# Performance work log

Measured on AMD Instinct MI355X. Metric: run time of the kernel, lower is better.

Reference implementation:

```python
import jax, jax.numpy as jnp
import numpy as np

N = 50000
E = 800000
T = 5            # towers
F = 10           # in_num / F_in per tower (divide_input=False)
F_OUT = 2        # out_channels // towers
G = 64           # number of graphs in the batch
L = 2            # conv layers
BN_EPS = 1e-5
STD_EPS = 1e-5


def setup_inputs() -> dict:
    key = jax.random.key(0)
    ks = jax.random.split(key, 24)
    s = 0.1
    inp = {
        'x': jax.random.normal(ks[0], (N, F), jnp.float32),
        'edge_emb': jax.random.normal(ks[1], (4, F), jnp.float32) * s,
        'mlp1_w1': jax.random.normal(ks[2], (F, 5), jnp.float32) * s,
        'mlp1_b1': jnp.zeros((5,), jnp.float32),
        'mlp1_w2': jax.random.normal(ks[3], (5, F), jnp.float32) * s,
        'mlp1_b2': jnp.zeros((F,), jnp.float32),
        'enc_w': jax.random.normal(ks[4], (L, F, F), jnp.float32) * s,
        'enc_b': jnp.zeros((L, F), jnp.float32),
        'pre_w': jax.random.normal(ks[5], (L, T, 3 * F, F), jnp.float32) * s,
        'pre_b': jnp.zeros((L, T, F), jnp.float32),
        'post_w': jax.random.normal(ks[6], (L, T, 13 * F, F_OUT), jnp.float32) * s,
        'post_b': jnp.zeros((L, T, F_OUT), jnp.float32),
        'lin_w': jax.random.normal(ks[7], (L, F, F), jnp.float32) * s,
        'lin_b': jnp.zeros((L, F), jnp.float32),
        'bn_gamma': jnp.ones((L, F), jnp.float32),
        'bn_beta': jnp.zeros((L, F), jnp.float32),
        'mlp2_w1': jax.random.normal(ks[8], (F, 5), jnp.float32) * s,
        'mlp2_b1': jnp.zeros((5,), jnp.float32),
        'mlp2_w2': jax.random.normal(ks[9], (5, 1), jnp.float32) * s,
        'mlp2_b2': jnp.zeros((1,), jnp.float32),
        'edge_index': jax.random.randint(ks[10], (2, E), 0, N, jnp.int64),
        'edge_attr': jax.random.randint(ks[11], (E,), 0, 4, jnp.int64),
        'batch': jnp.sort(jax.random.randint(ks[12], (N,), 0, G, jnp.int64)),
    }
    return inp


def reference(x, edge_emb, mlp1_w1, mlp1_b1, mlp1_w2, mlp1_b2,
              enc_w, enc_b, pre_w, pre_b, post_w, post_b, lin_w, lin_b,
              bn_gamma, bn_beta, mlp2_w1, mlp2_b1, mlp2_w2, mlp2_b2,
              edge_index, edge_attr, batch):
    src, dst = edge_index[0], edge_index[1]
    # mlp1: 10 -> 5 -> 10
    h = jax.nn.relu(x @ mlp1_w1 + mlp1_b1) @ mlp1_w2 + mlp1_b2  # [N, F]
    ea = edge_emb[edge_attr]  # [E, F] edge embedding lookup

    # in-degree at target nodes, PNA degree statistics
    deg = jax.ops.segment_sum(jnp.ones((src.shape[0],), h.dtype), dst, num_segments=N)
    d = jnp.clip(deg, 1.0)
    avg_log = jnp.mean(jnp.log(deg + 1.0))  # avg_deg['log'] from degree distribution
    log_d = jnp.log(d + 1.0)
    amp = (log_d / avg_log)[:, None, None]
    att = (avg_log / log_d)[:, None, None]
    has_in = (deg > 0)[:, None, None]
    inv_d = (1.0 / d)[:, None, None]

    for l in range(L):
        e = ea @ enc_w[l] + enc_b[l]  # [E, F]
        # message = pre_nn(cat(x_i, x_j, edge_attr)) per tower (x shared across towers)
        msg_in = jnp.concatenate([h[dst], h[src], e], axis=-1)  # [E, 3F]
        m = jnp.einsum('ef,tfo->eto', msg_in, pre_w[l]) + pre_b[l]  # [E, T, F]
        mean = jax.ops.segment_sum(m, dst, num_segments=N) * inv_d
        mean2 = jax.ops.segment_sum(m * m, dst, num_segments=N) * inv_d
        std = jnp.sqrt(jax.nn.relu(mean2 - mean * mean) + STD_EPS)
        mn = jnp.where(has_in, jax.ops.segment_min(m, dst, num_segments=N), 0.0)
        mx = jnp.where(has_in, jax.ops.segment_max(m, dst, num_segments=N), 0.0)
        agg = jnp.concatenate([mean, mn, mx, std], axis=-1)  # [N, T, 4F]
        agg = jnp.concatenate([agg, agg * amp, agg * att], axis=-1)  # [N, T, 12F]
        xt = jnp.broadcast_to(h[:, None, :], (h.shape[0], T, F))
        o = jnp.concatenate([xt, agg], axis=-1)  # [N, T, 13F]
        o = jnp.einsum('ntf,tfo->nto', o, post_w[l]) + post_b[l]  # [N, T, F_OUT]
        o = o.reshape(o.shape[0], T * F_OUT) @ lin_w[l] + lin_b[l]  # [N, F]
        # train-mode BatchNorm over nodes
        mu = jnp.mean(o, axis=0)
        var = jnp.var(o, axis=0)
        o = (o - mu) / jnp.sqrt(var + BN_EPS) * bn_gamma[l] + bn_beta[l]
        h = jax.nn.relu(o)

    g = jax.ops.segment_sum(h, batch, num_segments=G)  # global_add_pool -> [G, F]
    out = jax.nn.relu(g @ mlp2_w1 + mlp2_b1) @ mlp2_w2 + mlp2_b2  # [G, 1]
    return out
```

## Files before the change

kernel.cpp:

```cpp
#include <hip/hip_runtime.h>
#include <hip/hip_fp16.h>
#include <math.h>

#define N_NODES 50000
#define N_EDGES 800000
#define G_GRAPHS 64
#define BSTRIDE 64
#define CPAD 16
#define UROW 64
#define SENPK (N_NODES * 128)

#define WAVE_SYNC() asm volatile("s_waitcnt lgkmcnt(0)" ::: "memory")
#define RFL(v) __builtin_amdgcn_readfirstlane(v)

__global__ void k_zero(int* __restrict__ cnt) {
  int n = blockIdx.x * 256 + threadIdx.x;
  if (n < N_NODES) cnt[n * CPAD] = 0;
}

__global__ __launch_bounds__(256) void k_front(
    const float* __restrict__ x,
    const float* __restrict__ w1, const float* __restrict__ b1,
    const float* __restrict__ w2, const float* __restrict__ b2,
    float* __restrict__ h,
    int* __restrict__ cnt,
    float* __restrict__ bn_part, float* __restrict__ g,
    float* __restrict__ avg_log,
    const float* __restrict__ edge_emb,
    const float* __restrict__ enc_w, const float* __restrict__ enc_b,
    const float* __restrict__ pre_w, float* __restrict__ encm,
    __half* __restrict__ u,
    const int* __restrict__ src, const int* __restrict__ dst,
    const int* __restrict__ attr, int* __restrict__ epk) {
  __shared__ float eo[2][4][10];
  __shared__ float sw[500];
  int tid = threadIdx.x;
  int gid = blockIdx.x * 256 + tid;

  int ed = dst[gid];
  int es = src[gid];
  int ea = attr[gid];
  int rk = atomicAdd(&cnt[ed * CPAD], 1);

  if (gid < 1280) bn_part[gid] = 0.f;
  if (gid < G_GRAPHS * 10) g[gid] = 0.f;
  if (gid == 0) avg_log[0] = 0.f;
  { int z = gid - N_NODES; if (z >= 0 && z < UROW) u[N_NODES * UROW + z] = __float2half(0.f); }

  bool act = gid < N_NODES;
  float hr[10];
  if (act) {
    const float2* xp = (const float2*)(x + gid * 10);
    float xv[10];
#pragma unroll
    for (int k = 0; k < 5; k++) { float2 v = xp[k]; xv[2 * k] = v.x; xv[2 * k + 1] = v.y; }
    float hid[5];
#pragma unroll
    for (int j = 0; j < 5; j++) {
      float a = b1[j];
#pragma unroll
      for (int k = 0; k < 10; k++) a += xv[k] * w1[k * 5 + j];
      hid[j] = fmaxf(a, 0.f);
    }
#pragma unroll
    for (int f = 0; f < 10; f++) {
      float a = b2[f];
#pragma unroll
      for (int j = 0; j < 5; j++) a += hid[j] * w2[j * 10 + f];
      hr[f] = a;
      h[gid * 10 + f] = a;
    }
  }

  for (int j = tid; j < 500; j += 256) {
    int t = j / 100, k = (j / 10) % 10, f = j % 10;
    sw[j] = pre_w[(t * 30 + 10 + k) * 10 + f];
  }

  if (rk < BSTRIDE) epk[ed * BSTRIDE + rk] = es * 128 + ea;

  if (blockIdx.x == 0) {
    for (int i = tid; i < 80; i += 256) {
      int l = i / 40; int a = (i / 10) % 4; int k = i % 10;
      float s = enc_b[l * 10 + k];
      for (int j = 0; j < 10; j++) s += edge_emb[a * 10 + j] * enc_w[(l * 10 + j) * 10 + k];
      eo[l][a][k] = s;
    }
  }
  __syncthreads();
  if (blockIdx.x == 0) {
    for (int i = tid; i < 400; i += 256) {
      int l = i / 200; int a = (i / 50) % 4; int t = (i / 10) % 5; int f = i % 10;
      float s = 0.f;
      for (int k = 0; k < 10; k++) s += eo[l][a][k] * pre_w[((l * 5 + t) * 30 + 20 + k) * 10 + f];
      encm[i] = s;
    }
  }

  if (act) {
    __half2* up = (__half2*)(u + (size_t)gid * UROW);
#pragma unroll
    for (int c0 = 0; c0 < 25; c0++) {
      int ca = 2 * c0, cb = 2 * c0 + 1;
      int ta = ca / 10, fa = ca % 10, tb = cb / 10, fb = cb % 10;
      float a = 0.f, b = 0.f;
#pragma unroll
      for (int k = 0; k < 10; k++) {
        a += hr[k] * sw[ta * 100 + fa + k * 10];
        b += hr[k] * sw[tb * 100 + fb + k * 10];
      }
      up[c0] = __floats2half2_rn(a, b);
    }
  }
}

__global__ void k_avg(const int* __restrict__ cnt, float* __restrict__ avg_log,
                      int* __restrict__ epk) {
  __shared__ float ws[4];
  int tid = threadIdx.x;
  float acc = 0.f;
  for (int n = blockIdx.x * 256 + tid; n < N_NODES; n += gridDim.x * 256) {
    int dg = cnt[n * CPAD];
    acc += __logf((float)dg + 1.f);
    int dd = dg < BSTRIDE ? dg : BSTRIDE;
    int end = dd + 8 < BSTRIDE ? dd + 8 : BSTRIDE;
    for (int j = dd; j < end; j++) epk[n * BSTRIDE + j] = SENPK;
  }
#pragma unroll
  for (int d = 32; d >= 1; d >>= 1) acc += __shfl_down(acc, d, 64);
  if ((tid & 63) == 0) ws[tid >> 6] = acc;
  __syncthreads();
  if (tid == 0) atomicAdd(avg_log, ws[0] + ws[1] + ws[2] + ws[3]);
}

__global__ __launch_bounds__(256) void k_conv(
    const float* __restrict__ h,
    const __half* __restrict__ u,
    const float* __restrict__ pre_w_l,
    const float* __restrict__ pre_b_l,
    const float* __restrict__ post_w_l,
    const float* __restrict__ post_b_l,
    const float* __restrict__ lin_w_l,
    const float* __restrict__ lin_b_l,
    const float* __restrict__ encm_l,
    const int* __restrict__ cnt,
    const int* __restrict__ epk,
    const float* __restrict__ avg_log_p,
    float* __restrict__ o_buf,
    float* __restrict__ bn_part)
{
  __shared__ float sW[1300];
  __shared__ float sLin[100];
  __shared__ float sLb[10];
  __shared__ float sPb[10];
  __shared__ float sP[4][100];
  __shared__ float sO[4][10];
  __shared__ float bnS[10], bnQ[10];

  int tid = threadIdx.x;
  int wid = RFL(tid >> 6);
  int lane = tid & 63;
  for (int i = tid; i < 1300; i += 256) sW[i] = post_w_l[i];
  for (int i = tid; i < 100; i += 256) sLin[i] = lin_w_l[i];
  if (tid < 10) {
    sLb[tid] = lin_b_l[tid];
    sPb[tid] = post_b_l[tid];
    bnS[tid] = 0.f; bnQ[tid] = 0.f;
  }
  __syncthreads();

  int f = lane % 10;
  int t = (lane < 50) ? (lane / 10) : 4;
  int c50 = t * 10 + f;
  const char* ub = (const char*)u;
  int c50_2 = c50 * 2;
  float wdst[10];
#pragma unroll
  for (int k = 0; k < 10; k++) wdst[k] = pre_w_l[(t * 30 + k) * 10 + f];
  float em0 = encm_l[c50];
  float em1 = encm_l[50 + c50];
  float em2 = encm_l[100 + c50];
  float em3 = encm_l[150 + c50];
  float preb = pre_b_l[c50];
  float avg_log = avg_log_p[0] * (1.f / N_NODES);

  int n = blockIdx.x * 4 + wid;
  float bnSv = 0.f, bnQv = 0.f;

#define PRE(US, AS, IDX) { int sp_ = __builtin_amdgcn_readlane(pk, (IDX) & 63); \
    AS = sp_ & 3; \
    US = __half2float(*(const __half*)(ub + (sp_ & ~7) + c50_2)); }
#define PROC(US, AS) { float m_ = ((AS & 2) ? ((AS & 1) ? bem3 : bem2) : ((AS & 1) ? bem1 : bem0)) + US; \
    sum += m_; sq = fmaf(m_, m_, sq); mnv = fminf(mnv, m_); mxv = fmaxf(mxv, m_); }

  if (n < N_NODES) {
    int deg = RFL(cnt[n * CPAD]);
    if (deg > BSTRIDE) deg = BSTRIDE;
    int pk = epk[n * BSTRIDE + lane];

    const float* hn = h + n * 10;
    float2 d0 = *(const float2*)hn;
    float2 d1 = *(const float2*)(hn + 2);
    float2 d2 = *(const float2*)(hn + 4);
    float2 d3 = *(const float2*)(hn + 6);
    float2 d4 = *(const float2*)(hn + 8);
    float xf = hn[f];

    float base = preb
      + d0.x * wdst[0] + d0.y * wdst[1] + d1.x * wdst[2] + d1.y * wdst[3]
      + d2.x * wdst[4] + d2.y * wdst[5] + d3.x * wdst[6] + d3.y * wdst[7]
      + d4.x * wdst[8] + d4.y * wdst[9];
    float bem0 = base + em0, bem1 = base + em1, bem2 = base + em2, bem3 = base + em3;

    float sum = 0.f, sq = 0.f, mnv = INFINITY, mxv = -INFINITY;
    {
      float u0, u1, u2, u3, u4, u5, u6, u7;
      int a0, a1, a2, a3, a4, a5, a6, a7;
      PRE(u0, a0, 0) PRE(u1, a1, 1) PRE(u2, a2, 2) PRE(u3, a3, 3)
      PRE(u4, a4, 4) PRE(u5, a5, 5) PRE(u6, a6, 6) PRE(u7, a7, 7)
      int full = deg & ~7;
      int jb = 0;
      for (; jb < full; jb += 8) {
        PROC(u0, a0) PRE(u0, a0, jb + 8)
        PROC(u1, a1) PRE(u1, a1, jb + 9)
        PROC(u2, a2) PRE(u2, a2, jb + 10)
        PROC(u3, a3) PRE(u3, a3, jb + 11)
        PROC(u4, a4) PRE(u4, a4, jb + 12)
        PROC(u5, a5) PRE(u5, a5, jb + 13)
        PROC(u6, a6) PRE(u6, a6, jb + 14)
        PROC(u7, a7) PRE(u7, a7, jb + 15)
      }
      if (jb + 0 < deg) PROC(u0, a0)
      if (jb + 1 < deg) PROC(u1, a1)
      if (jb + 2 < deg) PROC(u2, a2)
      if (jb + 3 < deg) PROC(u3, a3)
      if (jb + 4 < deg) PROC(u4, a4)
      if (jb + 5 < deg) PROC(u5, a5)
      if (jb + 6 < deg) PROC(u6, a6)
    }

    float degf = (float)deg;
    float d = fmaxf(degf, 1.f);
    float inv = 1.f / d;
    float mean = sum * inv;
    float var = sq * inv - mean * mean;
    float stdv = sqrtf(fmaxf(var, 0.f) + 1e-5f);
    if (deg == 0) { mnv = 0.f; mxv = 0.f; }
    float log_d = logf(d + 1.f);
    float amp = log_d / avg_log;
    float att = avg_log / log_d;

    float vv[13];
    vv[0] = xf;
    vv[1] = mean;       vv[2] = mnv;        vv[3] = mxv;        vv[4] = stdv;
    vv[5] = mean * amp; vv[6] = mnv * amp;  vv[7] = mxv * amp;  vv[8] = stdv * amp;
    vv[9] = mean * att; vv[10] = mnv * att; vv[11] = mxv * att; vv[12] = stdv * att;
    float p0 = 0.f, p1 = 0.f;
#pragma unroll
    for (int j = 0; j < 13; j++) {
      const float2 w = *(const float2*)&sW[t * 260 + (f + 10 * j) * 2];
      p0 += vv[j] * w.x; p1 += vv[j] * w.y;
    }
    if (lane < 50) *(float2*)&sP[wid][c50 * 2] = make_float2(p0, p1);
    WAVE_SYNC();
    if (lane < 10) {
      int tt = lane >> 1, c = lane & 1;
      float o = sPb[lane];
#pragma unroll
      for (int ff = 0; ff < 10; ff++) o += sP[wid][(tt * 10 + ff) * 2 + c];
      sO[wid][lane] = o;
    }
    WAVE_SYNC();
    if (lane < 10) {
      float r = sLb[lane];
#pragma unroll
      for (int j = 0; j < 10; j++) r += sO[wid][j] * sLin[j * 10 + lane];
      o_buf[n * 10 + lane] = r;
      bnSv = r; bnQv = r * r;
    }
  }
#undef PRE
#undef PROC

  if (lane < 10) {
    atomicAdd(&bnS[lane], bnSv);
    atomicAdd(&bnQ[lane], bnQv);
  }
  __syncthreads();
  if (tid < 20) {
    float v = (tid < 10) ? bnS[tid] : bnQ[tid - 10];
    atomicAdd(&bn_part[(blockIdx.x & 31) * 20 + tid], v);
  }
}

__global__ __launch_bounds__(256) void k_bnpool(
    const float* __restrict__ o_buf,
    const float* __restrict__ bn_part,
    const float* __restrict__ gamma, const float* __restrict__ beta,
    float* __restrict__ h,
    const int* __restrict__ batch, float* __restrict__ g,
    const float* __restrict__ pre_w_next, __half* __restrict__ u,
    int do_u, int do_pool) {
  __shared__ float sS[20];
  __shared__ float sMu[10], sInv[10];
  __shared__ float pool[8][10];
  __shared__ float hrow[25][10];
  __shared__ float sw[500];
  __shared__ int g0s;
  int tid = threadIdx.x;
  int n0 = blockIdx.x * 25;
  if (do_u) {
    for (int j = tid; j < 500; j += 256) {
      int t = j / 100, k = (j / 10) % 10, f = j % 10;
      sw[j] = pre_w_next[(t * 30 + 10 + k) * 10 + f];
    }
  }
  if (tid < 20) {
    float s = 0.f;
    for (int j = 0; j < 32; j++) s += bn_part[j * 20 + tid];
    sS[tid] = s;
  }
  if (tid < 80) pool[tid / 10][tid % 10] = 0.f;
  if (tid == 0) g0s = batch[n0];
  __syncthreads();
  if (tid < 10) {
    float mu = sS[tid] * (1.f / N_NODES);
    float var = sS[10 + tid] * (1.f / N_NODES) - mu * mu;
    sMu[tid] = mu;
    sInv[tid] = 1.f / sqrtf(fmaxf(var, 0.f) + 1e-5f);
  }
  __syncthreads();
  if (tid < 250) {
    int dn = tid / 10, f = tid % 10;
    int n = n0 + dn;
    int i = n * 10 + f;
    float o = (o_buf[i] - sMu[f]) * sInv[f] * gamma[f] + beta[f];
    float r = fmaxf(o, 0.f);
    h[i] = r;
    hrow[dn][f] = r;
    if (do_pool) {
      int dg = batch[n] - g0s;
      if (dg < 8) atomicAdd(&pool[dg][f], r);
      else atomicAdd(&g[(g0s + dg) * 10 + f], r);
    }
  }
  __syncthreads();
  if (do_u && tid < 250) {
#pragma unroll
    for (int it = 0; it < 5; it++) {
      int j = tid + it * 250;
      int node = j / 50, c = j % 50;
      int t = c / 10, f2 = c % 10;
      float acc = 0.f;
#pragma unroll
      for (int k = 0; k < 10; k++) acc += hrow[node][k] * sw[t * 100 + f2 + k * 10];
      u[(size_t)(n0 + node) * UROW + c] = __float2half_rn(acc);
    }
  }
  if (do_pool) {
    __syncthreads();
    if (tid < 80) {
      float v = pool[tid / 10][tid % 10];
      if (v != 0.f) atomicAdd(&g[(g0s + tid / 10) * 10 + tid % 10], v);
    }
  }
}

__global__ void k_mlp2(const float* __restrict__ g,
                       const float* __restrict__ w1, const float* __restrict__ b1,
                       const float* __restrict__ w2, const float* __restrict__ b2,
                       float* __restrict__ out) {
  int b = threadIdx.x;
  if (b >= G_GRAPHS) return;
  float gv[10];
#pragma unroll
  for (int k = 0; k < 10; k++) gv[k] = g[b * 10 + k];
  float acc = b2[0];
#pragma unroll
  for (int j = 0; j < 5; j++) {
    float a = b1[j];
#pragma unroll
    for (int k = 0; k < 10; k++) a += gv[k] * w1[k * 5 + j];
    acc += fmaxf(a, 0.f) * w2[j];
  }
  out[b] = acc;
}

extern "C" void kernel_launch(void* const* d_in, const int* in_sizes, int n_in,
                              void* d_out, int out_size, void* d_ws, size_t ws_size,
                              hipStream_t stream) {
  const float* x        = (const float*)d_in[0];
  const float* edge_emb = (const float*)d_in[1];
  const float* m1w1 = (const float*)d_in[2];
  const float* m1b1 = (const float*)d_in[3];
  const float* m1w2 = (const float*)d_in[4];
  const float* m1b2 = (const float*)d_in[5];
  const float* enc_w = (const float*)d_in[6];
  const float* enc_b = (const float*)d_in[7];
  const float* pre_w = (const float*)d_in[8];
  const float* pre_b = (const float*)d_in[9];
  const float* post_w = (const float*)d_in[10];
  const float* post_b = (const float*)d_in[11];
  const float* lin_w = (const float*)d_in[12];
  const float* lin_b = (const float*)d_in[13];
  const float* bn_g = (const float*)d_in[14];
  const float* bn_b = (const float*)d_in[15];
  const float* m2w1 = (const float*)d_in[16];
  const float* m2b1 = (const float*)d_in[17];
  const float* m2w2 = (const float*)d_in[18];
  const float* m2b2 = (const float*)d_in[19];
  const int* edge_index = (const int*)d_in[20];
  const int* edge_attr  = (const int*)d_in[21];
  const int* batch      = (const int*)d_in[22];
  const int* src  = edge_index;
  const int* dstp = edge_index + N_EDGES;

  char* ws = (char*)d_ws;
  size_t off = 0;
  auto alloc = [&](size_t bytes) {
    void* p = ws + off;
    off += (bytes + 255) & ~(size_t)255;
    return p;
  };
  float*  h       = (float*)alloc(N_NODES * 10 * sizeof(float));
  float*  o_buf   = (float*)alloc(N_NODES * 10 * sizeof(float));
  __half* u       = (__half*)alloc((size_t)(N_NODES + 1) * UROW * sizeof(__half));
  int*    cnt     = (int*)alloc((size_t)N_NODES * CPAD * sizeof(int));
  int*    epk     = (int*)alloc((size_t)N_NODES * BSTRIDE * sizeof(int));
  float*  encm    = (float*)alloc(400 * sizeof(float));
  float*  avg_log = (float*)alloc(16);
  float*  bn_part = (float*)alloc(2 * 32 * 20 * sizeof(float));
  float*  g       = (float*)alloc(G_GRAPHS * 10 * sizeof(float));

  k_zero<<<(N_NODES + 255) / 256, 256, 0, stream>>>(cnt);

  k_front<<<N_EDGES / 256, 256, 0, stream>>>(x, m1w1, m1b1, m1w2, m1b2, h,
                                             cnt, bn_part, g, avg_log,
                                             edge_emb, enc_w, enc_b, pre_w, encm, u,
                                             src, dstp, edge_attr, epk);
  k_avg<<<64, 256, 0, stream>>>(cnt, avg_log, epk);

  for (int l = 0; l < 2; l++) {
    k_conv<<<N_NODES / 4, 256, 0, stream>>>(
        h, u, pre_w + l * 1500, pre_b + l * 50, post_w + l * 1300, post_b + l * 10,
        lin_w + l * 100, lin_b + l * 10, encm + l * 200,
        cnt, epk, avg_log, o_buf, bn_part + l * 640);
    k_bnpool<<<N_NODES / 25, 256, 0, stream>>>(
        o_buf, bn_part + l * 640, bn_g + l * 10, bn_b + l * 10, h, batch, g,
        pre_w + 1500, u, l == 0, l == 1);
  }
  k_mlp2<<<1, 64, 0, stream>>>(g, m2w1, m2b1, m2w2, m2b2, (float*)d_out);
}
```

Baseline: 293.3 us.

## Stage neighbor u-rows into LDS with per-lane vector loads before aggregation

```diff
diff --git a/kernel.cpp b/kernel.cpp
--- a/kernel.cpp
+++ b/kernel.cpp
@@ -8,7 +8,7 @@
 #define BSTRIDE 64
 #define CPAD 16
 #define UROW 64
-#define SENPK (N_NODES * 128)
+#define LROW 144
 
 #define WAVE_SYNC() asm volatile("s_waitcnt lgkmcnt(0)" ::: "memory")
 #define RFL(v) __builtin_amdgcn_readfirstlane(v)
@@ -45,7 +45,6 @@
   if (gid < 1280) bn_part[gid] = 0.f;
   if (gid < G_GRAPHS * 10) g[gid] = 0.f;
   if (gid == 0) avg_log[0] = 0.f;
-  { int z = gid - N_NODES; if (z >= 0 && z < UROW) u[N_NODES * UROW + z] = __float2half(0.f); }
 
   bool act = gid < N_NODES;
   float hr[10];
@@ -114,18 +113,12 @@
   }
 }
 
-__global__ void k_avg(const int* __restrict__ cnt, float* __restrict__ avg_log,
-                      int* __restrict__ epk) {
+__global__ void k_avg(const int* __restrict__ cnt, float* __restrict__ avg_log) {
   __shared__ float ws[4];
   int tid = threadIdx.x;
   float acc = 0.f;
-  for (int n = blockIdx.x * 256 + tid; n < N_NODES; n += gridDim.x * 256) {
-    int dg = cnt[n * CPAD];
-    acc += __logf((float)dg + 1.f);
-    int dd = dg < BSTRIDE ? dg : BSTRIDE;
-    int end = dd + 8 < BSTRIDE ? dd + 8 : BSTRIDE;
-    for (int j = dd; j < end; j++) epk[n * BSTRIDE + j] = SENPK;
-  }
+  for (int n = blockIdx.x * 256 + tid; n < N_NODES; n += gridDim.x * 256)
+    acc += __logf((float)cnt[n * CPAD] + 1.f);
 #pragma unroll
   for (int d = 32; d >= 1; d >>= 1) acc += __shfl_down(acc, d, 64);
   if ((tid & 63) == 0) ws[tid >> 6] = acc;
@@ -156,6 +149,7 @@
   __shared__ float sP[4][100];
   __shared__ float sO[4][10];
   __shared__ float bnS[10], bnQ[10];
+  __shared__ __align__(16) char ldsu[4][32 * LROW];
 
   int tid = threadIdx.x;
   int wid = RFL(tid >> 6);
@@ -187,16 +181,12 @@
   int n = blockIdx.x * 4 + wid;
   float bnSv = 0.f, bnQv = 0.f;
 
-#define PRE(US, AS, IDX) { int sp_ = __builtin_amdgcn_readlane(pk, (IDX) & 63); \
-    AS = sp_ & 3; \
-    US = __half2float(*(const __half*)(ub + (sp_ & ~7) + c50_2)); }
-#define PROC(US, AS) { float m_ = ((AS & 2) ? ((AS & 1) ? bem3 : bem2) : ((AS & 1) ? bem1 : bem0)) + US; \
-    sum += m_; sq = fmaf(m_, m_, sq); mnv = fminf(mnv, m_); mxv = fmaxf(mxv, m_); }
-
   if (n < N_NODES) {
     int deg = RFL(cnt[n * CPAD]);
     if (deg > BSTRIDE) deg = BSTRIDE;
     int pk = epk[n * BSTRIDE + lane];
+    const char* rb = ub + (pk & ~7);
+    char* lw = ldsu[wid];
 
     const float* hn = h + n * 10;
     float2 d0 = *(const float2*)hn;
@@ -213,30 +203,62 @@
     float bem0 = base + em0, bem1 = base + em1, bem2 = base + em2, bem3 = base + em3;
 
     float sum = 0.f, sq = 0.f, mnv = INFINITY, mxv = -INFINITY;
-    {
-      float u0, u1, u2, u3, u4, u5, u6, u7;
-      int a0, a1, a2, a3, a4, a5, a6, a7;
-      PRE(u0, a0, 0) PRE(u1, a1, 1) PRE(u2, a2, 2) PRE(u3, a3, 3)
-      PRE(u4, a4, 4) PRE(u5, a5, 5) PRE(u6, a6, 6) PRE(u7, a7, 7)
-      int full = deg & ~7;
-      int jb = 0;
-      for (; jb < full; jb += 8) {
-        PROC(u0, a0) PRE(u0, a0, jb + 8)
-        PROC(u1, a1) PRE(u1, a1, jb + 9)
-        PROC(u2, a2) PRE(u2, a2, jb + 10)
-        PROC(u3, a3) PRE(u3, a3, jb + 11)
-        PROC(u4, a4) PRE(u4, a4, jb + 12)
-        PROC(u5, a5) PRE(u5, a5, jb + 13)
-        PROC(u6, a6) PRE(u6, a6, jb + 14)
-        PROC(u7, a7) PRE(u7, a7, jb + 15)
+
+    int cend = deg < 32 ? deg : 32;
+    if (lane < cend) {
+      float4 v0 = *(const float4*)(rb +  0);
+      float4 v1 = *(const float4*)(rb + 16);
+      float4 v2 = *(const float4*)(rb + 32);
+      float4 v3 = *(const float4*)(rb + 48);
+      float4 v4 = *(const float4*)(rb + 64);
+      float4 v5 = *(const float4*)(rb + 80);
+      float4 v6 = *(const float4*)(rb + 96);
+      char* lp = lw + lane * LROW;
+      *(float4*)(lp +  0) = v0;
+      *(float4*)(lp + 16) = v1;
+      *(float4*)(lp + 32) = v2;
+      *(float4*)(lp + 48) = v3;
+      *(float4*)(lp + 64) = v4;
+      *(float4*)(lp + 80) = v5;
+      *(float4*)(lp + 96) = v6;
+    }
+    WAVE_SYNC();
+#pragma unroll 4
+    for (int jj = 0; jj < cend; jj++) {
+      int sp_ = __builtin_amdgcn_readlane(pk, jj);
+      int as = sp_ & 3;
+      float us = __half2float(*(const __half*)(lw + jj * LROW + c50_2));
+      float m_ = ((as & 2) ? ((as & 1) ? bem3 : bem2) : ((as & 1) ? bem1 : bem0)) + us;
+      sum += m_; sq = fmaf(m_, m_, sq); mnv = fminf(mnv, m_); mxv = fmaxf(mxv, m_);
+    }
+    if (deg > 32) {
+      int cend2 = deg - 32;
+      if (lane >= 32 && lane < 32 + cend2) {
+        float4 v0 = *(const float4*)(rb +  0);
+        float4 v1 = *(const float4*)(rb + 16);
+        float4 v2 = *(const float4*)(rb + 32);
+        float4 v3 = *(const float4*)(rb + 48);
+        float4 v4 = *(const float4*)(rb + 64);
+        float4 v5 = *(const float4*)(rb + 80);
+        float4 v6 = *(const float4*)(rb + 96);
+        char* lp = lw + (lane - 32) * LROW;
+        *(float4*)(lp +  0) = v0;
+        *(float4*)(lp + 16) = v1;
+        *(float4*)(lp + 32) = v2;
+        *(float4*)(lp + 48) = v3;
+        *(float4*)(lp + 64) = v4;
+        *(float4*)(lp + 80) = v5;
+        *(float4*)(lp + 96) = v6;
       }
-      if (jb + 0 < deg) PROC(u0, a0)
-      if (jb + 1 < deg) PROC(u1, a1)
-      if (jb + 2 < deg) PROC(u2, a2)
-      if (jb + 3 < deg) PROC(u3, a3)
-      if (jb + 4 < deg) PROC(u4, a4)
-      if (jb + 5 < deg) PROC(u5, a5)
-      if (jb + 6 < deg) PROC(u6, a6)
+      WAVE_SYNC();
+#pragma unroll 4
+      for (int jj = 0; jj < cend2; jj++) {
+        int sp_ = __builtin_amdgcn_readlane(pk, 32 + jj);
+        int as = sp_ & 3;
+        float us = __half2float(*(const __half*)(lw + jj * LROW + c50_2));
+        float m_ = ((as & 2) ? ((as & 1) ? bem3 : bem2) : ((as & 1) ? bem1 : bem0)) + us;
+        sum += m_; sq = fmaf(m_, m_, sq); mnv = fminf(mnv, m_); mxv = fmaxf(mxv, m_);
+      }
     }
 
     float degf = (float)deg;
@@ -279,8 +301,6 @@
       bnSv = r; bnQv = r * r;
     }
   }
-#undef PRE
-#undef PROC
 
   if (lane < 10) {
     atomicAdd(&bnS[lane], bnSv);
@@ -438,7 +458,7 @@
                                              cnt, bn_part, g, avg_log,
                                              edge_emb, enc_w, enc_b, pre_w, encm, u,
                                              src, dstp, edge_attr, epk);
-  k_avg<<<64, 256, 0, stream>>>(cnt, avg_log, epk);
+  k_avg<<<64, 256, 0, stream>>>(cnt, avg_log);
 
   for (int l = 0; l < 2; l++) {
     k_conv<<<N_NODES / 4, 256, 0, stream>>>(
```

Result: slower. 313.9 us (+7.0%).

## Shard per-node edge counters across block groups to reduce atomic contention

Applied to the files above, without the earlier changes.

```diff
diff --git a/kernel.cpp b/kernel.cpp
--- a/kernel.cpp
+++ b/kernel.cpp
@@ -6,16 +6,18 @@
 #define N_EDGES 800000
 #define G_GRAPHS 64
 #define BSTRIDE 64
-#define CPAD 16
+#define SHARDS 8
+#define SLOTS 12
+#define EPKW 96
 #define UROW 64
 #define SENPK (N_NODES * 128)
 
 #define WAVE_SYNC() asm volatile("s_waitcnt lgkmcnt(0)" ::: "memory")
 #define RFL(v) __builtin_amdgcn_readfirstlane(v)
 
-__global__ void k_zero(int* __restrict__ cnt) {
-  int n = blockIdx.x * 256 + threadIdx.x;
-  if (n < N_NODES) cnt[n * CPAD] = 0;
+__global__ void k_zero(int* __restrict__ cnt2) {
+  int i = blockIdx.x * 256 + threadIdx.x;
+  if (i < SHARDS * N_NODES) cnt2[i] = 0;
 }
 
 __global__ __launch_bounds__(256) void k_front(
@@ -23,7 +25,7 @@
     const float* __restrict__ w1, const float* __restrict__ b1,
     const float* __restrict__ w2, const float* __restrict__ b2,
     float* __restrict__ h,
-    int* __restrict__ cnt,
+    int* __restrict__ cnt2,
     float* __restrict__ bn_part, float* __restrict__ g,
     float* __restrict__ avg_log,
     const float* __restrict__ edge_emb,
@@ -36,16 +38,17 @@
   __shared__ float sw[500];
   int tid = threadIdx.x;
   int gid = blockIdx.x * 256 + tid;
+  int sh = blockIdx.x & (SHARDS - 1);
 
   int ed = dst[gid];
   int es = src[gid];
   int ea = attr[gid];
-  int rk = atomicAdd(&cnt[ed * CPAD], 1);
+  int rk = atomicAdd(&cnt2[sh * N_NODES + ed], 1);
 
   if (gid < 1280) bn_part[gid] = 0.f;
   if (gid < G_GRAPHS * 10) g[gid] = 0.f;
   if (gid == 0) avg_log[0] = 0.f;
-  { int z = gid - N_NODES; if (z >= 0 && z < UROW) u[N_NODES * UROW + z] = __float2half(0.f); }
+  { int z = gid - N_NODES; if (z >= 0 && z < UROW) u[(size_t)N_NODES * UROW + z] = __float2half(0.f); }
 
   bool act = gid < N_NODES;
   float hr[10];
@@ -77,7 +80,7 @@
     sw[j] = pre_w[(t * 30 + 10 + k) * 10 + f];
   }
 
-  if (rk < BSTRIDE) epk[ed * BSTRIDE + rk] = es * 128 + ea;
+  if (rk < SLOTS) epk[ed * EPKW + sh * SLOTS + rk] = es * 128 + ea;
 
   if (blockIdx.x == 0) {
     for (int i = tid; i < 80; i += 256) {
@@ -114,17 +117,19 @@
   }
 }
 
-__global__ void k_avg(const int* __restrict__ cnt, float* __restrict__ avg_log,
-                      int* __restrict__ epk) {
+__global__ void k_avg(const int* __restrict__ cnt2, float* __restrict__ avg_log) {
   __shared__ float ws[4];
   int tid = threadIdx.x;
   float acc = 0.f;
   for (int n = blockIdx.x * 256 + tid; n < N_NODES; n += gridDim.x * 256) {
-    int dg = cnt[n * CPAD];
+    int dg = 0;
+#pragma unroll
+    for (int s2 = 0; s2 < SHARDS; s2++) {
+      int cc = cnt2[s2 * N_NODES + n];
+      dg += (cc < SLOTS ? cc : SLOTS);
+    }
+    if (dg > BSTRIDE) dg = BSTRIDE;
     acc += __logf((float)dg + 1.f);
-    int dd = dg < BSTRIDE ? dg : BSTRIDE;
-    int end = dd + 8 < BSTRIDE ? dd + 8 : BSTRIDE;
-    for (int j = dd; j < end; j++) epk[n * BSTRIDE + j] = SENPK;
   }
 #pragma unroll
   for (int d = 32; d >= 1; d >>= 1) acc += __shfl_down(acc, d, 64);
@@ -143,7 +148,7 @@
     const float* __restrict__ lin_w_l,
     const float* __restrict__ lin_b_l,
     const float* __restrict__ encm_l,
-    const int* __restrict__ cnt,
+    const int* __restrict__ cnt2,
     const int* __restrict__ epk,
     const float* __restrict__ avg_log_p,
     float* __restrict__ o_buf,
@@ -194,9 +199,30 @@
     sum += m_; sq = fmaf(m_, m_, sq); mnv = fminf(mnv, m_); mxv = fmaxf(mxv, m_); }
 
   if (n < N_NODES) {
-    int deg = RFL(cnt[n * CPAD]);
-    if (deg > BSTRIDE) deg = BSTRIDE;
-    int pk = epk[n * BSTRIDE + lane];
+    int cs, oa[8];
+    int dg = 0;
+#pragma unroll
+    for (int s2 = 0; s2 < SHARDS; s2++) {
+      int cc = cnt2[s2 * N_NODES + n];
+      cc = cc < SLOTS ? cc : SLOTS;
+      oa[s2] = dg; dg += cc;
+    }
+    int deg = dg < BSTRIDE ? dg : BSTRIDE;
+    int nb = n * EPKW;
+    int raw0 = epk[nb + lane];
+    int raw1 = (lane < EPKW - 64) ? epk[nb + 64 + lane] : 0;
+    int shard = 0;
+#pragma unroll
+    for (int q = 1; q < SHARDS; q++) shard += (lane >= oa[q]) ? 1 : 0;
+    int D = 0;
+#pragma unroll
+    for (int q = 1; q < SHARDS; q++) D = (shard == q) ? (q * SLOTS - oa[q]) : D;
+    int ri = lane + D;
+    int plo = __shfl(raw0, ri & 63, 64);
+    int phi = __shfl(raw1, (ri - 64) & 63, 64);
+    int pk = (ri < 64) ? plo : phi;
+    pk = (lane < deg) ? pk : SENPK;
+    (void)cs;
 
     const float* hn = h + n * 10;
     float2 d0 = *(const float2*)hn;
@@ -425,26 +451,26 @@
   float*  h       = (float*)alloc(N_NODES * 10 * sizeof(float));
   float*  o_buf   = (float*)alloc(N_NODES * 10 * sizeof(float));
   __half* u       = (__half*)alloc((size_t)(N_NODES + 1) * UROW * sizeof(__half));
-  int*    cnt     = (int*)alloc((size_t)N_NODES * CPAD * sizeof(int));
-  int*    epk     = (int*)alloc((size_t)N_NODES * BSTRIDE * sizeof(int));
+  int*    cnt2    = (int*)alloc((size_t)SHARDS * N_NODES * sizeof(int));
+  int*    epk     = (int*)alloc((size_t)N_NODES * EPKW * sizeof(int));
   float*  encm    = (float*)alloc(400 * sizeof(float));
   float*  avg_log = (float*)alloc(16);
   float*  bn_part = (float*)alloc(2 * 32 * 20 * sizeof(float));
   float*  g       = (float*)alloc(G_GRAPHS * 10 * sizeof(float));
 
-  k_zero<<<(N_NODES + 255) / 256, 256, 0, stream>>>(cnt);
+  k_zero<<<(SHARDS * N_NODES + 255) / 256, 256, 0, stream>>>(cnt2);
 
   k_front<<<N_EDGES / 256, 256, 0, stream>>>(x, m1w1, m1b1, m1w2, m1b2, h,
-                                             cnt, bn_part, g, avg_log,
+                                             cnt2, bn_part, g, avg_log,
                                              edge_emb, enc_w, enc_b, pre_w, encm, u,
                                              src, dstp, edge_attr, epk);
-  k_avg<<<64, 256, 0, stream>>>(cnt, avg_log, epk);
+  k_avg<<<64, 256, 0, stream>>>(cnt2, avg_log);
 
   for (int l = 0; l < 2; l++) {
     k_conv<<<N_NODES / 4, 256, 0, stream>>>(
         h, u, pre_w + l * 1500, pre_b + l * 50, post_w + l * 1300, post_b + l * 10,
         lin_w + l * 100, lin_b + l * 10, encm + l * 200,
-        cnt, epk, avg_log, o_buf, bn_part + l * 640);
+        cnt2, epk, avg_log, o_buf, bn_part + l * 640);
     k_bnpool<<<N_NODES / 25, 256, 0, stream>>>(
         o_buf, bn_part + l * 640, bn_g + l * 10, bn_b + l * 10, h, batch, g,
         pre_w + 1500, u, l == 0, l == 1);
```

Measured after the change: 296.2 us. About the same (+1.0%).

## Replace global atomic edge binning with two-pass shared-memory bucket sort

Applied to the files above, without the earlier changes.

```diff
diff --git a/kernel.cpp b/kernel.cpp
--- a/kernel.cpp
+++ b/kernel.cpp
@@ -6,24 +6,21 @@
 #define N_EDGES 800000
 #define G_GRAPHS 64
 #define BSTRIDE 64
-#define CPAD 16
 #define UROW 64
 #define SENPK (N_NODES * 128)
+#define SBLK 64
+#define EPB 12500
+#define NBUCK 1563
+#define SCAP 32
 
 #define WAVE_SYNC() asm volatile("s_waitcnt lgkmcnt(0)" ::: "memory")
 #define RFL(v) __builtin_amdgcn_readfirstlane(v)
-
-__global__ void k_zero(int* __restrict__ cnt) {
-  int n = blockIdx.x * 256 + threadIdx.x;
-  if (n < N_NODES) cnt[n * CPAD] = 0;
-}
 
 __global__ __launch_bounds__(256) void k_front(
     const float* __restrict__ x,
     const float* __restrict__ w1, const float* __restrict__ b1,
     const float* __restrict__ w2, const float* __restrict__ b2,
     float* __restrict__ h,
-    int* __restrict__ cnt,
     float* __restrict__ bn_part, float* __restrict__ g,
     float* __restrict__ avg_log,
     const float* __restrict__ edge_emb,
@@ -31,55 +28,21 @@
     const float* __restrict__ pre_w, float* __restrict__ encm,
     __half* __restrict__ u,
     const int* __restrict__ src, const int* __restrict__ dst,
-    const int* __restrict__ attr, int* __restrict__ epk) {
+    const int* __restrict__ attr,
+    int* __restrict__ rec,
+    int* __restrict__ cntmat) {
+  __shared__ int hist[NBUCK];
   __shared__ float eo[2][4][10];
   __shared__ float sw[500];
-  int tid = threadIdx.x;
-  int gid = blockIdx.x * 256 + tid;
-
-  int ed = dst[gid];
-  int es = src[gid];
-  int ea = attr[gid];
-  int rk = atomicAdd(&cnt[ed * CPAD], 1);
-
-  if (gid < 1280) bn_part[gid] = 0.f;
-  if (gid < G_GRAPHS * 10) g[gid] = 0.f;
-  if (gid == 0) avg_log[0] = 0.f;
-  { int z = gid - N_NODES; if (z >= 0 && z < UROW) u[N_NODES * UROW + z] = __float2half(0.f); }
-
-  bool act = gid < N_NODES;
-  float hr[10];
-  if (act) {
-    const float2* xp = (const float2*)(x + gid * 10);
-    float xv[10];
-#pragma unroll
-    for (int k = 0; k < 5; k++) { float2 v = xp[k]; xv[2 * k] = v.x; xv[2 * k + 1] = v.y; }
-    float hid[5];
-#pragma unroll
-    for (int j = 0; j < 5; j++) {
-      float a = b1[j];
-#pragma unroll
-      for (int k = 0; k < 10; k++) a += xv[k] * w1[k * 5 + j];
-      hid[j] = fmaxf(a, 0.f);
-    }
-#pragma unroll
-    for (int f = 0; f < 10; f++) {
-      float a = b2[f];
-#pragma unroll
-      for (int j = 0; j < 5; j++) a += hid[j] * w2[j * 10 + f];
-      hr[f] = a;
-      h[gid * 10 + f] = a;
-    }
-  }
-
+  int tid = threadIdx.x, blk = blockIdx.x;
+  int gid = blk * 256 + tid;
+
+  for (int i = tid; i < NBUCK; i += 256) hist[i] = 0;
   for (int j = tid; j < 500; j += 256) {
     int t = j / 100, k = (j / 10) % 10, f = j % 10;
     sw[j] = pre_w[(t * 30 + 10 + k) * 10 + f];
   }
-
-  if (rk < BSTRIDE) epk[ed * BSTRIDE + rk] = es * 128 + ea;
-
-  if (blockIdx.x == 0) {
+  if (blk == 0) {
     for (int i = tid; i < 80; i += 256) {
       int l = i / 40; int a = (i / 10) % 4; int k = i % 10;
       float s = enc_b[l * 10 + k];
@@ -87,8 +50,61 @@
       eo[l][a][k] = s;
     }
   }
-  __syncthreads();
-  if (blockIdx.x == 0) {
+  if (gid < 1280) bn_part[gid] = 0.f;
+  if (gid < G_GRAPHS * 10) g[gid] = 0.f;
+  if (gid == 0) avg_log[0] = 0.f;
+  if (gid < UROW) u[(size_t)N_NODES * UROW + gid] = __float2half(0.f);
+  __syncthreads();
+
+  int ebase = blk * EPB;
+  for (int i = tid; i < EPB; i += 256) {
+    int e = ebase + i;
+    int d = dst[e];
+    int s = src[e];
+    int a = attr[e];
+    int bkt = d >> 5;
+    int r = atomicAdd(&hist[bkt], 1);
+    if (r < SCAP) rec[(bkt * SBLK + blk) * SCAP + r] = (s * 128 + a) | ((d & 31) << 23);
+  }
+
+  for (int node = gid; node < N_NODES; node += SBLK * 256) {
+    const float2* xp = (const float2*)(x + node * 10);
+    float xv[10];
+#pragma unroll
+    for (int k = 0; k < 5; k++) { float2 v = xp[k]; xv[2 * k] = v.x; xv[2 * k + 1] = v.y; }
+    float hid[5];
+#pragma unroll
+    for (int j = 0; j < 5; j++) {
+      float a = b1[j];
+#pragma unroll
+      for (int k = 0; k < 10; k++) a += xv[k] * w1[k * 5 + j];
+      hid[j] = fmaxf(a, 0.f);
+    }
+    float hr[10];
+#pragma unroll
+    for (int f = 0; f < 10; f++) {
+      float a = b2[f];
+#pragma unroll
+      for (int j = 0; j < 5; j++) a += hid[j] * w2[j * 10 + f];
+      hr[f] = a;
+      h[node * 10 + f] = a;
+    }
+    __half2* up = (__half2*)(u + (size_t)node * UROW);
+#pragma unroll
+    for (int c0 = 0; c0 < 25; c0++) {
+      int ca = 2 * c0, cb = 2 * c0 + 1;
+      int ta = ca / 10, fa = ca % 10, tb = cb / 10, fb = cb % 10;
+      float a = 0.f, b = 0.f;
+#pragma unroll
+      for (int k = 0; k < 10; k++) {
+        a += hr[k] * sw[ta * 100 + fa + k * 10];
+        b += hr[k] * sw[tb * 100 + fb + k * 10];
+      }
+      up[c0] = __floats2half2_rn(a, b);
+    }
+  }
+
+  if (blk == 0) {
     for (int i = tid; i < 400; i += 256) {
       int l = i / 200; int a = (i / 50) % 4; int t = (i / 10) % 5; int f = i % 10;
       float s = 0.f;
@@ -96,41 +112,51 @@
       encm[i] = s;
     }
   }
-
-  if (act) {
-    __half2* up = (__half2*)(u + (size_t)gid * UROW);
-#pragma unroll
-    for (int c0 = 0; c0 < 25; c0++) {
-      int ca = 2 * c0, cb = 2 * c0 + 1;
-      int ta = ca / 10, fa = ca % 10, tb = cb / 10, fb = cb % 10;
-      float a = 0.f, b = 0.f;
-#pragma unroll
-      for (int k = 0; k < 10; k++) {
-        a += hr[k] * sw[ta * 100 + fa + k * 10];
-        b += hr[k] * sw[tb * 100 + fb + k * 10];
-      }
-      up[c0] = __floats2half2_rn(a, b);
-    }
-  }
-}
-
-__global__ void k_avg(const int* __restrict__ cnt, float* __restrict__ avg_log,
-                      int* __restrict__ epk) {
-  __shared__ float ws[4];
-  int tid = threadIdx.x;
+  __syncthreads();
+  for (int b2 = tid; b2 < NBUCK; b2 += 256) {
+    int c = hist[b2];
+    cntmat[b2 * SBLK + blk] = c < SCAP ? c : SCAP;
+  }
+}
+
+__global__ __launch_bounds__(256) void k_bucket(
+    const int* __restrict__ rec, const int* __restrict__ cntmat,
+    int* __restrict__ epk, int* __restrict__ cnt,
+    float* __restrict__ avg_log) {
+  __shared__ int lc[SBLK];
+  __shared__ int lcnt[32];
+  int tid = threadIdx.x, b = blockIdx.x;
+  if (tid < SBLK) lc[tid] = cntmat[b * SBLK + tid];
+  if (tid < 32) lcnt[tid] = 0;
+  __syncthreads();
+  const int* rb = rec + (size_t)b * SBLK * SCAP;
+#pragma unroll
+  for (int p = 0; p < 8; p++) {
+    int t2 = tid + p * 256;
+    int j = t2 >> 5, i = t2 & 31;
+    if (i < lc[j]) {
+      int r = rb[t2];
+      int d5 = r >> 23;
+      int rank = atomicAdd(&lcnt[d5], 1);
+      if (rank < BSTRIDE) epk[((b << 5) + d5) * BSTRIDE + rank] = r & 0x7FFFFF;
+    }
+  }
+  __syncthreads();
   float acc = 0.f;
-  for (int n = blockIdx.x * 256 + tid; n < N_NODES; n += gridDim.x * 256) {
-    int dg = cnt[n * CPAD];
-    acc += __logf((float)dg + 1.f);
-    int dd = dg < BSTRIDE ? dg : BSTRIDE;
-    int end = dd + 8 < BSTRIDE ? dd + 8 : BSTRIDE;
-    for (int j = dd; j < end; j++) epk[n * BSTRIDE + j] = SENPK;
-  }
-#pragma unroll
-  for (int d = 32; d >= 1; d >>= 1) acc += __shfl_down(acc, d, 64);
-  if ((tid & 63) == 0) ws[tid >> 6] = acc;
-  __syncthreads();
-  if (tid == 0) atomicAdd(avg_log, ws[0] + ws[1] + ws[2] + ws[3]);
+  if (tid < 32) {
+    int node = (b << 5) + tid;
+    if (node < N_NODES) {
+      int dg = lcnt[tid];
+      cnt[node] = dg;
+      if (dg > BSTRIDE) dg = BSTRIDE;
+      acc = __logf((float)dg + 1.f);
+    }
+  }
+  if (tid < 64) {
+#pragma unroll
+    for (int d = 32; d >= 1; d >>= 1) acc += __shfl_down(acc, d, 64);
+    if (tid == 0) atomicAdd(avg_log, acc);
+  }
 }
 
 __global__ __launch_bounds__(256) void k_conv(
@@ -194,9 +220,10 @@
     sum += m_; sq = fmaf(m_, m_, sq); mnv = fminf(mnv, m_); mxv = fmaxf(mxv, m_); }
 
   if (n < N_NODES) {
-    int deg = RFL(cnt[n * CPAD]);
+    int deg = RFL(cnt[n]);
     if (deg > BSTRIDE) deg = BSTRIDE;
     int pk = epk[n * BSTRIDE + lane];
+    pk = (lane < deg) ? pk : SENPK;
 
     const float* hn = h + n * 10;
     float2 d0 = *(const float2*)hn;
@@ -425,20 +452,20 @@
   float*  h       = (float*)alloc(N_NODES * 10 * sizeof(float));
   float*  o_buf   = (float*)alloc(N_NODES * 10 * sizeof(float));
   __half* u       = (__half*)alloc((size_t)(N_NODES + 1) * UROW * sizeof(__half));
-  int*    cnt     = (int*)alloc((size_t)N_NODES * CPAD * sizeof(int));
+  int*    cnt     = (int*)alloc((size_t)N_NODES * sizeof(int));
   int*    epk     = (int*)alloc((size_t)N_NODES * BSTRIDE * sizeof(int));
+  int*    rec     = (int*)alloc((size_t)NBUCK * SBLK * SCAP * sizeof(int));
+  int*    cntmat  = (int*)alloc((size_t)NBUCK * SBLK * sizeof(int));
   float*  encm    = (float*)alloc(400 * sizeof(float));
   float*  avg_log = (float*)alloc(16);
   float*  bn_part = (float*)alloc(2 * 32 * 20 * sizeof(float));
   float*  g       = (float*)alloc(G_GRAPHS * 10 * sizeof(float));
 
-  k_zero<<<(N_NODES + 255) / 256, 256, 0, stream>>>(cnt);
-
-  k_front<<<N_EDGES / 256, 256, 0, stream>>>(x, m1w1, m1b1, m1w2, m1b2, h,
-                                             cnt, bn_part, g, avg_log,
-                                             edge_emb, enc_w, enc_b, pre_w, encm, u,
-                                             src, dstp, edge_attr, epk);
-  k_avg<<<64, 256, 0, stream>>>(cnt, avg_log, epk);
+  k_front<<<SBLK, 256, 0, stream>>>(x, m1w1, m1b1, m1w2, m1b2, h,
+                                    bn_part, g, avg_log,
+                                    edge_emb, enc_w, enc_b, pre_w, encm, u,
+                                    src, dstp, edge_attr, rec, cntmat);
+  k_bucket<<<NBUCK, 256, 0, stream>>>(rec, cntmat, epk, cnt, avg_log);
 
   for (int l = 0; l < 2; l++) {
     k_conv<<<N_NODES / 4, 256, 0, stream>>>(
```

New measurement: 301.8 us. 2.9% more time.
